# Kernel tuning notes

Hardware: AMD Instinct MI355X
Metric: run time of the kernel (lower is better)

## Reference

```python
import jax, jax.numpy as jnp
import numpy as np
from jax import lax

N, C_IN, L = 32, 256, 4096
C_OUT, K, GROUPS = 256, 9, 4
C_DIM, PAD, STRIDE = 128, 4, 1


def setup_inputs() -> dict:
    key = jax.random.key(0)
    k1, k2, k3, k4, k5 = jax.random.split(key, 5)
    x = jax.random.normal(k1, (N, C_IN, L), dtype=jnp.float32)
    c = jax.random.normal(k2, (N, C_DIM), dtype=jnp.float32)
    weight = jax.random.normal(k3, (C_OUT, C_IN // GROUPS, K), dtype=jnp.float32)
    c_weight = jax.random.normal(k4, (C_OUT, C_DIM), dtype=jnp.float32)
    bias = jax.random.normal(k5, (C_OUT,), dtype=jnp.float32)
    return {"x": x, "c": c, "weight": weight, "c_weight": c_weight, "bias": bias}


def reference(x, c, weight, c_weight, bias):
    # Grouped conv1d: equivalent to the unfold+per-group matmul in the torch code.
    # dims: x (N, C_in, L), weight (C_out, C_in/groups, K) -> out (N, C_out, L_out)
    out = lax.conv_general_dilated(
        x, weight,
        window_strides=(STRIDE,),
        padding=[(PAD, PAD)],
        dimension_numbers=("NCH", "OIH", "NCH"),
        feature_group_count=GROUPS,
    )
    # Concat-path context: cat([patches, c]) @ cat([W, cW]).T == conv(x) + c @ cW.T,
    # with the context term broadcast over all temporal positions.
    ctx = jnp.einsum("nd,od->no", c, c_weight)  # (N, C_out)
    out = out + ctx[:, :, None] + bias[None, :, None]
    return out
```

## Files before the change

kernel.cpp:

```cpp
#include <hip/hip_runtime.h>
#include <hip/hip_bf16.h>

#define NB     32
#define CIN    256
#define LIN    4096
#define COUT   256
#define KW     9
#define NGRP   4
#define CDIM   128
#define CPG    64
#define LT     128
#define NTILE  (LIN / LT)
#define NROWS  (LT + 8)
#define RP     68
#define WF_ELEMS (4*4*9*2*64*8)

typedef __attribute__((ext_vector_type(8))) short short8;
typedef __attribute__((ext_vector_type(4))) short short4v;
typedef __attribute__((ext_vector_type(4))) float float4v;
typedef __attribute__((ext_vector_type(4))) unsigned short ushort4v;

__global__ void pack_weights(const float* __restrict__ w, __hip_bfloat16* __restrict__ wF) {
    int tid = blockIdx.x * blockDim.x + threadIdx.x;
    if (tid >= WF_ELEMS) return;
    int j    = tid & 7;
    int lane = (tid >> 3) & 63;
    int rest = tid >> 9;
    int chunk = rest & 1;  rest >>= 1;
    int k     = rest % 9;  rest /= 9;
    int co16  = rest & 3;
    int g     = rest >> 2;
    int co = g * CPG + co16 * 16 + (lane & 15);
    int ci = chunk * 32 + (lane >> 4) * 8 + j;
    wF[tid] = __float2bfloat16(w[(co * CPG + ci) * KW + k]);
}

__global__ __launch_bounds__(256) void ctx_kernel(const float* __restrict__ c,
                                                  const float* __restrict__ cw,
                                                  const float* __restrict__ bias,
                                                  float* __restrict__ ctxb) {
    int gw   = (blockIdx.x * 256 + threadIdx.x) >> 6;
    int lane = threadIdx.x & 63;
    int n  = gw >> 8;
    int co = gw & 255;
    float s = c[n * CDIM + lane]      * cw[co * CDIM + lane]
            + c[n * CDIM + 64 + lane] * cw[co * CDIM + 64 + lane];
    #pragma unroll
    for (int off = 32; off; off >>= 1) s += __shfl_down(s, off);
    if (lane == 0) ctxb[gw] = s + bias[co];
}

__global__ __launch_bounds__(256, 5) void conv_mfma(
    const float* __restrict__ x, const __hip_bfloat16* __restrict__ wF,
    const float* __restrict__ ctxb, float* __restrict__ out)
{
    __shared__ unsigned short sx[NROWS * RP];
    __shared__ float sctx[CPG];

    const int bx = blockIdx.x;
    const int t  = bx & 31;
    const int g  = (bx >> 5) & 3;
    const int n  = bx >> 7;
    const int l0 = t * LT;
    const int tid = threadIdx.x;
    const int lane = tid & 63;
    const int wv   = tid >> 6;

    if (tid < CPG) sctx[tid] = ctxb[n * COUT + g * CPG + tid];

    const float* xb = x + ((size_t)(n * CIN + g * CPG)) * LIN;

    {
        int q4  = 1 + (lane & 15);
        int cqb = 4 * wv + (lane >> 4);
        #pragma unroll
        for (int i = 0; i < 2; ++i, q4 += 16) {
            int lg = l0 - 4 + 4 * q4;
            float4v v[4];
            #pragma unroll
            for (int j = 0; j < 4; ++j)
                v[j] = *(const float4v*)(xb + (size_t)(4 * cqb + j) * LIN + lg);
            int row = 4 * q4;
            #pragma unroll
            for (int d = 0; d < 4; ++d) {
                ushort4v p;
                #pragma unroll
                for (int j = 0; j < 4; ++j)
                    p[j] = __builtin_bit_cast(unsigned short, __float2bfloat16(v[j][d]));
                *(ushort4v*)(&sx[(row + d) * RP + 4 * cqb]) = p;
            }
        }
    }
    if (tid < 32) {
        int head = (tid < 16);
        int q4 = head ? 0 : (LT / 4 + 1);
        int cq = tid & 15;
        int lg = l0 - 4 + 4 * q4;
        bool ok = head ? (t > 0) : (t < NTILE - 1);
        float4v v[4];
        #pragma unroll
        for (int j = 0; j < 4; ++j)
            v[j] = ok ? *(const float4v*)(xb + (size_t)(4 * cq + j) * LIN + lg)
                      : (float4v){0.f, 0.f, 0.f, 0.f};
        int row = 4 * q4;
        #pragma unroll
        for (int d = 0; d < 4; ++d) {
            ushort4v p;
            #pragma unroll
            for (int j = 0; j < 4; ++j)
                p[j] = __builtin_bit_cast(unsigned short, __float2bfloat16(v[j][d]));
            *(ushort4v*)(&sx[(row + d) * RP + 4 * cq]) = p;
        }
    }
    __syncthreads();

    const int r  = lane & 15;
    const int q  = lane >> 4;
    const int wl = wv * 32;

    float4v acc[4][2];
    #pragma unroll
    for (int a = 0; a < 4; ++a)
        #pragma unroll
        for (int b = 0; b < 2; ++b)
            acc[a][b] = (float4v){0.f, 0.f, 0.f, 0.f};

    const short8* wFp = (const short8*)wF;

    #pragma unroll
    for (int k = 0; k < KW; ++k) {
        #pragma unroll
        for (int chunk = 0; chunk < 2; ++chunk) {
            short8 bfrag[2];
            #pragma unroll
            for (int l16 = 0; l16 < 2; ++l16) {
                int row = wl + l16 * 16 + r + k;
                int base = row * RP + chunk * 32 + q * 8;
                short4v lo = *(const short4v*)(&sx[base]);
                short4v hi = *(const short4v*)(&sx[base + 4]);
                bfrag[l16] = __builtin_shufflevector(lo, hi, 0, 1, 2, 3, 4, 5, 6, 7);
            }
            #pragma unroll
            for (int co16 = 0; co16 < 4; ++co16) {
                short8 af = wFp[(((g * 4 + co16) * 9 + k) * 2 + chunk) * 64 + lane];
                #pragma unroll
                for (int l16 = 0; l16 < 2; ++l16)
                    acc[co16][l16] = __builtin_amdgcn_mfma_f32_16x16x32_bf16(
                        af, bfrag[l16], acc[co16][l16], 0, 0, 0);
            }
        }
    }

    float* ob = out + ((size_t)(n * COUT + g * CPG)) * LIN + l0 + wl;
    #pragma unroll
    for (int co16 = 0; co16 < 4; ++co16) {
        #pragma unroll
        for (int reg = 0; reg < 4; ++reg) {
            int co_l = co16 * 16 + q * 4 + reg;
            float add = sctx[co_l];
            #pragma unroll
            for (int l16 = 0; l16 < 2; ++l16) {
                ob[(size_t)co_l * LIN + l16 * 16 + r] = acc[co16][l16][reg] + add;
            }
        }
    }
}

extern "C" void kernel_launch(void* const* d_in, const int* in_sizes, int n_in,
                              void* d_out, int out_size, void* d_ws, size_t ws_size,
                              hipStream_t stream) {
    const float* x    = (const float*)d_in[0];
    const float* c    = (const float*)d_in[1];
    const float* w    = (const float*)d_in[2];
    const float* cw   = (const float*)d_in[3];
    const float* bias = (const float*)d_in[4];
    float* out = (float*)d_out;

    __hip_bfloat16* wF = (__hip_bfloat16*)d_ws;
    float* ctxb = (float*)((char*)d_ws + (size_t)WF_ELEMS * 2);

    pack_weights<<<(WF_ELEMS + 255) / 256, 256, 0, stream>>>(w, wF);
    ctx_kernel<<<(NB * COUT * 64) / 256, 256, 0, stream>>>(c, cw, bias, ctxb);
    conv_mfma<<<NB * NGRP * NTILE, 256, 0, stream>>>(x, wF, ctxb, out);
}
```

Measured before the change: 276.5 us.

## Assign each wave a 16-channel output slice with register-resident weights

```diff
diff --git a/kernel.cpp b/kernel.cpp
--- a/kernel.cpp
+++ b/kernel.cpp
@@ -50,7 +50,7 @@
     if (lane == 0) ctxb[gw] = s + bias[co];
 }
 
-__global__ __launch_bounds__(256, 5) void conv_mfma(
+__global__ __launch_bounds__(256, 3) void conv_mfma(
     const float* __restrict__ x, const __hip_bfloat16* __restrict__ wF,
     const float* __restrict__ ctxb, float* __restrict__ out)
 {
@@ -68,101 +68,94 @@
 
     if (tid < CPG) sctx[tid] = ctxb[n * COUT + g * CPG + tid];
 
+    const short8* wFp = (const short8*)wF;
+    const short8* wbase = wFp + (size_t)((g * 4 + wv) * 9 * 2) * 64 + lane;
+    short8 wreg[2 * KW];
+    #pragma unroll
+    for (int i = 0; i < 2 * KW; ++i) wreg[i] = wbase[(size_t)i * 64];
+
     const float* xb = x + ((size_t)(n * CIN + g * CPG)) * LIN;
 
-    {
-        int q4  = 1 + (lane & 15);
-        int cqb = 4 * wv + (lane >> 4);
+    const int q4  = 1 + (lane & 15);
+    const int cqb = 4 * wv + (lane >> 4);
+    float4v v[8];
+    #pragma unroll
+    for (int i = 0; i < 2; ++i) {
+        int lg = l0 - 4 + 4 * (q4 + 16 * i);
         #pragma unroll
-        for (int i = 0; i < 2; ++i, q4 += 16) {
-            int lg = l0 - 4 + 4 * q4;
-            float4v v[4];
+        for (int j = 0; j < 4; ++j)
+            v[i * 4 + j] = *(const float4v*)(xb + (size_t)(4 * cqb + j) * LIN + lg);
+    }
+    float4v hv[4] = {{0.f,0.f,0.f,0.f},{0.f,0.f,0.f,0.f},{0.f,0.f,0.f,0.f},{0.f,0.f,0.f,0.f}};
+    const int hq4 = (tid < 16) ? 0 : (LT / 4 + 1);
+    const int hcq = tid & 15;
+    if (tid < 32) {
+        bool ok = (tid < 16) ? (t > 0) : (t < NTILE - 1);
+        int lg = l0 - 4 + 4 * hq4;
+        if (ok) {
             #pragma unroll
             for (int j = 0; j < 4; ++j)
-                v[j] = *(const float4v*)(xb + (size_t)(4 * cqb + j) * LIN + lg);
-            int row = 4 * q4;
-            #pragma unroll
-            for (int d = 0; d < 4; ++d) {
-                ushort4v p;
-                #pragma unroll
-                for (int j = 0; j < 4; ++j)
-                    p[j] = __builtin_bit_cast(unsigned short, __float2bfloat16(v[j][d]));
-                *(ushort4v*)(&sx[(row + d) * RP + 4 * cqb]) = p;
-            }
+                hv[j] = *(const float4v*)(xb + (size_t)(4 * hcq + j) * LIN + lg);
         }
     }
-    if (tid < 32) {
-        int head = (tid < 16);
-        int q4 = head ? 0 : (LT / 4 + 1);
-        int cq = tid & 15;
-        int lg = l0 - 4 + 4 * q4;
-        bool ok = head ? (t > 0) : (t < NTILE - 1);
-        float4v v[4];
-        #pragma unroll
-        for (int j = 0; j < 4; ++j)
-            v[j] = ok ? *(const float4v*)(xb + (size_t)(4 * cq + j) * LIN + lg)
-                      : (float4v){0.f, 0.f, 0.f, 0.f};
-        int row = 4 * q4;
+    #pragma unroll
+    for (int i = 0; i < 2; ++i) {
+        int row = 4 * (q4 + 16 * i);
         #pragma unroll
         for (int d = 0; d < 4; ++d) {
             ushort4v p;
             #pragma unroll
             for (int j = 0; j < 4; ++j)
-                p[j] = __builtin_bit_cast(unsigned short, __float2bfloat16(v[j][d]));
-            *(ushort4v*)(&sx[(row + d) * RP + 4 * cq]) = p;
+                p[j] = __builtin_bit_cast(unsigned short, __float2bfloat16(v[i * 4 + j][d]));
+            *(ushort4v*)(&sx[(row + d) * RP + 4 * cqb]) = p;
+        }
+    }
+    if (tid < 32) {
+        int row = 4 * hq4;
+        #pragma unroll
+        for (int d = 0; d < 4; ++d) {
+            ushort4v p;
+            #pragma unroll
+            for (int j = 0; j < 4; ++j)
+                p[j] = __builtin_bit_cast(unsigned short, __float2bfloat16(hv[j][d]));
+            *(ushort4v*)(&sx[(row + d) * RP + 4 * hcq]) = p;
         }
     }
     __syncthreads();
 
-    const int r  = lane & 15;
-    const int q  = lane >> 4;
-    const int wl = wv * 32;
+    const int r = lane & 15;
+    const int q = lane >> 4;
 
-    float4v acc[4][2];
+    float4v acc[LT / 16];
     #pragma unroll
-    for (int a = 0; a < 4; ++a)
-        #pragma unroll
-        for (int b = 0; b < 2; ++b)
-            acc[a][b] = (float4v){0.f, 0.f, 0.f, 0.f};
-
-    const short8* wFp = (const short8*)wF;
+    for (int b = 0; b < LT / 16; ++b)
+        acc[b] = (float4v){0.f, 0.f, 0.f, 0.f};
 
     #pragma unroll
     for (int k = 0; k < KW; ++k) {
         #pragma unroll
-        for (int chunk = 0; chunk < 2; ++chunk) {
-            short8 bfrag[2];
+        for (int ch = 0; ch < 2; ++ch) {
+            short8 af = wreg[k * 2 + ch];
             #pragma unroll
-            for (int l16 = 0; l16 < 2; ++l16) {
-                int row = wl + l16 * 16 + r + k;
-                int base = row * RP + chunk * 32 + q * 8;
+            for (int l16 = 0; l16 < LT / 16; ++l16) {
+                int row = l16 * 16 + r + k;
+                int base = row * RP + ch * 32 + q * 8;
                 short4v lo = *(const short4v*)(&sx[base]);
                 short4v hi = *(const short4v*)(&sx[base + 4]);
-                bfrag[l16] = __builtin_shufflevector(lo, hi, 0, 1, 2, 3, 4, 5, 6, 7);
-            }
-            #pragma unroll
-            for (int co16 = 0; co16 < 4; ++co16) {
-                short8 af = wFp[(((g * 4 + co16) * 9 + k) * 2 + chunk) * 64 + lane];
-                #pragma unroll
-                for (int l16 = 0; l16 < 2; ++l16)
-                    acc[co16][l16] = __builtin_amdgcn_mfma_f32_16x16x32_bf16(
-                        af, bfrag[l16], acc[co16][l16], 0, 0, 0);
+                short8 bf = __builtin_shufflevector(lo, hi, 0, 1, 2, 3, 4, 5, 6, 7);
+                acc[l16] = __builtin_amdgcn_mfma_f32_16x16x32_bf16(af, bf, acc[l16], 0, 0, 0);
             }
         }
     }
 
-    float* ob = out + ((size_t)(n * COUT + g * CPG)) * LIN + l0 + wl;
+    float* ob = out + ((size_t)(n * COUT + g * CPG)) * LIN + l0;
     #pragma unroll
-    for (int co16 = 0; co16 < 4; ++co16) {
+    for (int rg = 0; rg < 4; ++rg) {
+        int co_l = wv * 16 + q * 4 + rg;
+        float add = sctx[co_l];
         #pragma unroll
-        for (int reg = 0; reg < 4; ++reg) {
-            int co_l = co16 * 16 + q * 4 + reg;
-            float add = sctx[co_l];
-            #pragma unroll
-            for (int l16 = 0; l16 < 2; ++l16) {
-                ob[(size_t)co_l * LIN + l16 * 16 + r] = acc[co16][l16][reg] + add;
-            }
-        }
+        for (int l16 = 0; l16 < LT / 16; ++l16)
+            ob[(size_t)co_l * LIN + l16 * 16 + r] = acc[l16][rg] + add;
     }
 }
 
```

Result: faster. 249.1 us (-9.9%).
